# Kernel tuning notes

Measured on AMD Instinct MI355X. Metric: run time of the kernel, lower is better.

The kernel has to match this reference:

```python
import jax, jax.numpy as jnp
import numpy as np

VOCAB = 32000
EMB = 512
HID = 512
MAX_LEN = 32
SOS = 1
PAD = 0


def setup_inputs() -> dict:
    key = jax.random.key(0)
    ks = jax.random.split(key, 9)
    s = 1.0 / np.sqrt(HID)
    emb = jax.random.normal(ks[0], (VOCAB, EMB), jnp.float32)
    emb = emb.at[PAD].set(0.0)  # padding_idx row is zeros
    return {
        "encoder_hidden": jax.random.normal(ks[1], (1, 64, HID), jnp.float32),
        "encoder_c": jax.random.normal(ks[2], (1, 64, HID), jnp.float32),
        "emb": emb,
        "W_ih": jax.random.uniform(ks[3], (4 * HID, EMB), jnp.float32, -s, s),
        "W_hh": jax.random.uniform(ks[4], (4 * HID, HID), jnp.float32, -s, s),
        "b_ih": jax.random.uniform(ks[5], (4 * HID,), jnp.float32, -s, s),
        "b_hh": jax.random.uniform(ks[6], (4 * HID,), jnp.float32, -s, s),
        "fc_w": jax.random.uniform(ks[7], (VOCAB, HID), jnp.float32, -s, s),
        "fc_b": jax.random.uniform(ks[8], (VOCAB,), jnp.float32, -s, s),
    }


def reference(encoder_hidden, encoder_c, emb, W_ih, W_hh, b_ih, b_hh, fc_w, fc_b):
    B = encoder_hidden.shape[1]
    h0 = encoder_hidden[0]  # [B,H] (num_layers == 1)
    c0 = encoder_c[0]
    tok0 = jnp.full((B,), SOS, jnp.int32)
    bias = b_ih + b_hh  # [4H]

    def step(carry, _):
        tok, h, c = carry
        x = emb[tok]  # [B,E] embedding gather
        gates = x @ W_ih.T + h @ W_hh.T + bias  # [B,4H]
        i, f, g, o = jnp.split(gates, 4, axis=-1)  # torch gate order i,f,g,o
        c = jax.nn.sigmoid(f) * c + jax.nn.sigmoid(i) * jnp.tanh(g)
        h = jax.nn.sigmoid(o) * jnp.tanh(c)
        logp = jax.nn.log_softmax(h @ fc_w.T + fc_b, axis=-1)  # [B,V]
        tok_next = jnp.argmax(logp, axis=-1).astype(jnp.int32)  # greedy topk(k=1)
        return (tok_next, h, c), logp

    (_, hT, _), logps = jax.lax.scan(step, (tok0, h0, c0), None, length=MAX_LEN + 1)
    decoder_outputs = jnp.transpose(logps, (1, 0, 2))  # [B, T, V]
    decoder_hidden = hT[None]  # [1, B, H]
    return decoder_outputs, decoder_hidden
```

## Files before the change

kernel.cpp:

```cpp
#include <hip/hip_runtime.h>
#include <math.h>

#define VOCABN 32000
#define HIDN 512
#define BN 64
#define TSTEPS 33
#define OUTROWS (TSTEPS * VOCABN)
#define NVBLK 1000
#define NVT 2000
#define GSLICE 8

typedef float f4 __attribute__((ext_vector_type(4)));
typedef __bf16 bf16x8 __attribute__((ext_vector_type(8)));
typedef unsigned short u16x8 __attribute__((ext_vector_type(8)));

__device__ __forceinline__ unsigned short f2bf_rn(float f) {
    unsigned int u = __builtin_bit_cast(unsigned int, f);
    u += 0x7FFFu + ((u >> 16) & 1u);
    return (unsigned short)(u >> 16);
}
__device__ __forceinline__ float bfbits2f(unsigned short s) {
    unsigned int u = ((unsigned int)s) << 16;
    return __builtin_bit_cast(float, u);
}
__device__ __forceinline__ float sigf(float x) { return 1.f / (1.f + expf(-x)); }
__device__ __forceinline__ void olmerge(float& m, float& s, int& idx,
                                        float mo, float so, int io) {
    float M = fmaxf(m, mo);
    s = s * __expf(m - M) + so * __expf(mo - M);
    idx = (mo > m) ? io : ((mo == m) ? (io < idx ? io : idx) : idx);
    m = M;
}

__global__ __launch_bounds__(256) void k_init(const float* __restrict__ eh,
                                              const float* __restrict__ ec,
                                              float* __restrict__ h,
                                              float* __restrict__ c,
                                              int* __restrict__ tok) {
    int i = blockIdx.x * 256 + threadIdx.x;
    if (i < BN * HIDN) { h[i] = eh[i]; c[i] = ec[i]; }
    if (i < BN) tok[i] = 1;
}

__global__ __launch_bounds__(256) void k_conv(const float* __restrict__ fc_w,
                                              unsigned short* __restrict__ whiP,
                                              unsigned short* __restrict__ wloP) {
    const int vt = blockIdx.x;
    const int tid = threadIdx.x;
    #pragma unroll
    for (int i = 0; i < 4; ++i) {
        const int s = tid + 256 * i;
        const int kc = s >> 6, lane = s & 63;
        const int v = vt * 16 + (lane & 15);
        const int k = kc * 32 + (lane >> 4) * 8;
        const float* src = fc_w + (size_t)v * 512 + k;
        f4 a = *(const f4*)src;
        f4 b = *(const f4*)(src + 4);
        u16x8 hi, lo;
        #pragma unroll
        for (int e = 0; e < 4; ++e) {
            unsigned short ha = f2bf_rn(a[e]);
            hi[e] = ha; lo[e] = f2bf_rn(a[e] - bfbits2f(ha));
            unsigned short hb = f2bf_rn(b[e]);
            hi[4 + e] = hb; lo[4 + e] = f2bf_rn(b[e] - bfbits2f(hb));
        }
        const size_t o = ((size_t)(vt * 16 + kc) * 64 + lane) * 8;
        *(u16x8*)&whiP[o] = hi;
        *(u16x8*)&wloP[o] = lo;
    }
}

__global__ __launch_bounds__(256) void k_gates(const float* __restrict__ W_ih,
                                               const float* __restrict__ W_hh,
                                               const float* __restrict__ emb,
                                               const float* __restrict__ h,
                                               const int* __restrict__ tok,
                                               float* __restrict__ part) {
    __shared__ float w_s[64][68];
    __shared__ float x_s[64][68];
    const int tid = threadIdx.x;
    const int j0 = (blockIdx.x & 31) * 64;
    const int ks = blockIdx.x >> 5;
    const int k0 = ks * 128;
    const int tx = tid & 15;
    const int ty = tid >> 4;
    const int r  = tid >> 2;
    const int cq = (tid & 3) * 16;

    float acc[4][4];
    #pragma unroll
    for (int i = 0; i < 4; ++i)
        #pragma unroll
        for (int j = 0; j < 4; ++j) acc[i][j] = 0.f;

    for (int kk = 0; kk < 128; kk += 64) {
        const int k = k0 + kk;
        __syncthreads();
        {
            const float* src = (k < 512) ? (W_ih + (size_t)(j0 + r) * 512 + k + cq)
                                         : (W_hh + (size_t)(j0 + r) * 512 + (k - 512) + cq);
            const f4* s4 = (const f4*)src;
            f4* d4 = (f4*)&w_s[r][cq];
            d4[0] = s4[0]; d4[1] = s4[1]; d4[2] = s4[2]; d4[3] = s4[3];
        }
        {
            const float* src = (k < 512) ? (emb + (size_t)tok[r] * 512 + k + cq)
                                         : (h + (size_t)r * 512 + (k - 512) + cq);
            const f4* s4 = (const f4*)src;
            f4* d4 = (f4*)&x_s[r][cq];
            d4[0] = s4[0]; d4[1] = s4[1]; d4[2] = s4[2]; d4[3] = s4[3];
        }
        __syncthreads();
        #pragma unroll 4
        for (int c4 = 0; c4 < 64; c4 += 4) {
            f4 wv[4], xv[4];
            #pragma unroll
            for (int jj = 0; jj < 4; ++jj) wv[jj] = *(const f4*)&w_s[16 * jj + tx][c4];
            #pragma unroll
            for (int bb = 0; bb < 4; ++bb) xv[bb] = *(const f4*)&x_s[16 * bb + ty][c4];
            #pragma unroll
            for (int e = 0; e < 4; ++e)
                #pragma unroll
                for (int bb = 0; bb < 4; ++bb)
                    #pragma unroll
                    for (int jj = 0; jj < 4; ++jj)
                        acc[bb][jj] += xv[bb][e] * wv[jj][e];
        }
    }
    #pragma unroll
    for (int bb = 0; bb < 4; ++bb) {
        const int b = 16 * bb + ty;
        #pragma unroll
        for (int jj = 0; jj < 4; ++jj)
            part[((size_t)(ks * 64 + b)) * 2048 + j0 + 16 * jj + tx] = acc[bb][jj];
    }
}

__global__ __launch_bounds__(256) void k_cell(const float* __restrict__ part,
                                              const float* __restrict__ b_ih,
                                              const float* __restrict__ b_hh,
                                              float* __restrict__ h,
                                              float* __restrict__ c,
                                              unsigned short* __restrict__ hhi,
                                              unsigned short* __restrict__ hlo) {
    const int e = blockIdx.x * 256 + threadIdx.x;
    const int b = e >> 9, u = e & 511;
    float g[4];
    #pragma unroll
    for (int gi = 0; gi < 4; ++gi) {
        const int j = gi * 512 + u;
        float s = b_ih[j] + b_hh[j];
        #pragma unroll
        for (int ks = 0; ks < GSLICE; ++ks) s += part[((size_t)(ks * 64 + b)) * 2048 + j];
        g[gi] = s;
    }
    const float ig = sigf(g[0]);
    const float fg = sigf(g[1]);
    const float gg = tanhf(g[2]);
    const float og = sigf(g[3]);
    const float cn = fg * c[e] + ig * gg;
    const float hn = og * tanhf(cn);
    c[e] = cn;
    h[e] = hn;
    const unsigned short hi = f2bf_rn(hn);
    hhi[e] = hi;
    hlo[e] = f2bf_rn(hn - bfbits2f(hi));
}

__global__ __launch_bounds__(256, 4) void k_logits(const unsigned short* __restrict__ whiP,
                                                   const unsigned short* __restrict__ wloP,
                                                   const float* __restrict__ fc_b,
                                                   const unsigned short* __restrict__ hhi,
                                                   const unsigned short* __restrict__ hlo,
                                                   float* __restrict__ outrow,
                                                   float* __restrict__ pm,
                                                   float* __restrict__ ps,
                                                   int* __restrict__ pi) {
    __shared__ float sacc[2][16][64];
    __shared__ float red_m[128];
    __shared__ float red_s[128];
    __shared__ int   red_i[128];

    const int tid  = threadIdx.x;
    const int w    = tid >> 6;
    const int lane = tid & 63;
    const int li   = lane & 15;
    const int lg   = lane >> 4;
    const int vtl  = w >> 1;
    const int kh   = w & 1;
    const int vt   = blockIdx.x * 2 + vtl;

    f4 acc[4];
    #pragma unroll
    for (int bf = 0; bf < 4; ++bf) acc[bf] = (f4){0.f, 0.f, 0.f, 0.f};

    const unsigned short* Ah = whiP + (size_t)vt * 8192 + kh * 4096 + lane * 8;
    const unsigned short* Al = wloP + (size_t)vt * 8192 + kh * 4096 + lane * 8;
    int boff[4];
    #pragma unroll
    for (int bf = 0; bf < 4; ++bf) boff[bf] = (li + 16 * bf) * 512 + kh * 256 + lg * 8;

    #pragma unroll 4
    for (int kc = 0; kc < 8; ++kc) {
        bf16x8 Avh = *(const bf16x8*)(Ah + kc * 512);
        bf16x8 Avl = *(const bf16x8*)(Al + kc * 512);
        #pragma unroll
        for (int bf = 0; bf < 4; ++bf) {
            bf16x8 Bh = *(const bf16x8*)&hhi[boff[bf] + kc * 32];
            bf16x8 Bl = *(const bf16x8*)&hlo[boff[bf] + kc * 32];
            acc[bf] = __builtin_amdgcn_mfma_f32_16x16x32_bf16(Avh, Bh, acc[bf], 0, 0, 0);
            acc[bf] = __builtin_amdgcn_mfma_f32_16x16x32_bf16(Avl, Bh, acc[bf], 0, 0, 0);
            acc[bf] = __builtin_amdgcn_mfma_f32_16x16x32_bf16(Avh, Bl, acc[bf], 0, 0, 0);
        }
    }

    if (kh == 1) {
        #pragma unroll
        for (int bf = 0; bf < 4; ++bf)
            #pragma unroll
            for (int rg = 0; rg < 4; ++rg)
                sacc[vtl][bf * 4 + rg][lane] = acc[bf][rg];
    }
    __syncthreads();

    if (kh == 0) {
        #pragma unroll
        for (int bf = 0; bf < 4; ++bf)
            #pragma unroll
            for (int rg = 0; rg < 4; ++rg)
                acc[bf][rg] += sacc[vtl][bf * 4 + rg][lane];

        const int vbase = vt * 16;
        const f4 bias = *(const f4*)&fc_b[vbase + lg * 4];

        #pragma unroll
        for (int bf = 0; bf < 4; ++bf) {
            f4 x = acc[bf] + bias;
            acc[bf] = x;
            const int b = li + 16 * bf;
            *(f4*)&outrow[(size_t)b * OUTROWS + vbase + lg * 4] = x;
        }

        #pragma unroll
        for (int bf = 0; bf < 4; ++bf) {
            float m = -1e30f; int idx = 0;
            #pragma unroll
            for (int rg = 0; rg < 4; ++rg) {
                float x = acc[bf][rg];
                if (x > m) { m = x; idx = vbase + lg * 4 + rg; }
            }
            float s = 0.f;
            #pragma unroll
            for (int rg = 0; rg < 4; ++rg) s += __expf(acc[bf][rg] - m);
            #pragma unroll
            for (int off = 16; off <= 32; off <<= 1) {
                float mo = __shfl_xor(m, off);
                float so = __shfl_xor(s, off);
                int   io = __shfl_xor(idx, off);
                olmerge(m, s, idx, mo, so, io);
            }
            if (lg == 0) {
                red_m[vtl * 64 + li + 16 * bf] = m;
                red_s[vtl * 64 + li + 16 * bf] = s;
                red_i[vtl * 64 + li + 16 * bf] = idx;
            }
        }
    }
    __syncthreads();
    if (tid < 64) {
        float m = red_m[tid]; float s = red_s[tid]; int idx = red_i[tid];
        olmerge(m, s, idx, red_m[64 + tid], red_s[64 + tid], red_i[64 + tid]);
        pm[blockIdx.x * 64 + tid] = m;
        ps[blockIdx.x * 64 + tid] = s;
        pi[blockIdx.x * 64 + tid] = idx;
    }
}

__global__ __launch_bounds__(256) void k_combine(const float* __restrict__ pm,
                                                 const float* __restrict__ ps,
                                                 const int* __restrict__ pi,
                                                 int* __restrict__ tok,
                                                 float* __restrict__ Lb, int t) {
    __shared__ float sm[256], ss[256];
    __shared__ int si[256];
    const int b = blockIdx.x;
    const int tid = threadIdx.x;
    float m = -1e30f, s = 0.f; int idx = 0;
    for (int blk = tid; blk < NVBLK; blk += 256)
        olmerge(m, s, idx, pm[blk * 64 + b], ps[blk * 64 + b], pi[blk * 64 + b]);
    sm[tid] = m; ss[tid] = s; si[tid] = idx;
    __syncthreads();
    for (int st = 128; st; st >>= 1) {
        if (tid < st) {
            float m0 = sm[tid], s0 = ss[tid]; int i0 = si[tid];
            olmerge(m0, s0, i0, sm[tid + st], ss[tid + st], si[tid + st]);
            sm[tid] = m0; ss[tid] = s0; si[tid] = i0;
        }
        __syncthreads();
    }
    if (tid == 0) { tok[b] = si[0]; Lb[t * 64 + b] = sm[0] + logf(ss[0]); }
}

__global__ __launch_bounds__(256) void k_sub(float* __restrict__ out,
                                             const float* __restrict__ Lb) {
    const int N4 = BN * OUTROWS / 4;
    for (int i4 = blockIdx.x * 256 + threadIdx.x; i4 < N4; i4 += gridDim.x * 256) {
        const int i = i4 * 4;
        const int b = i / OUTROWS;
        const int rem = i - b * OUTROWS;
        const int t = rem / VOCABN;
        f4 x = *(const f4*)&out[i];
        const float L = Lb[t * 64 + b];
        x[0] -= L; x[1] -= L; x[2] -= L; x[3] -= L;
        *(f4*)&out[i] = x;
    }
}

__global__ __launch_bounds__(256) void k_copyh(const float* __restrict__ h,
                                               float* __restrict__ dst) {
    int i = blockIdx.x * 256 + threadIdx.x;
    if (i < BN * HIDN) dst[i] = h[i];
}

__global__ __launch_bounds__(256) void k_logits_f32(const float* __restrict__ fc_w,
                                                    const float* __restrict__ fc_b,
                                                    const float* __restrict__ h,
                                                    float* __restrict__ outrow) {
    __shared__ float w_s[64][68];
    __shared__ float h_s[64][68];
    const int tid = threadIdx.x;
    const int v0 = blockIdx.x * 64;
    const int tx = tid & 15;
    const int ty = tid >> 4;
    const int r  = tid >> 2;
    const int cq = (tid & 3) * 16;

    float acc[4][4];
    #pragma unroll
    for (int i = 0; i < 4; ++i)
        #pragma unroll
        for (int j = 0; j < 4; ++j) acc[i][j] = 0.f;

    for (int k = 0; k < 512; k += 64) {
        __syncthreads();
        {
            const f4* s4 = (const f4*)(fc_w + (size_t)(v0 + r) * 512 + k + cq);
            f4* d4 = (f4*)&w_s[r][cq];
            d4[0] = s4[0]; d4[1] = s4[1]; d4[2] = s4[2]; d4[3] = s4[3];
        }
        {
            const f4* s4 = (const f4*)(h + (size_t)r * 512 + k + cq);
            f4* d4 = (f4*)&h_s[r][cq];
            d4[0] = s4[0]; d4[1] = s4[1]; d4[2] = s4[2]; d4[3] = s4[3];
        }
        __syncthreads();
        #pragma unroll 4
        for (int c4 = 0; c4 < 64; c4 += 4) {
            f4 wv[4], hv[4];
            #pragma unroll
            for (int vv = 0; vv < 4; ++vv) wv[vv] = *(const f4*)&w_s[16 * vv + tx][c4];
            #pragma unroll
            for (int bb = 0; bb < 4; ++bb) hv[bb] = *(const f4*)&h_s[16 * bb + ty][c4];
            #pragma unroll
            for (int e = 0; e < 4; ++e)
                #pragma unroll
                for (int bb = 0; bb < 4; ++bb)
                    #pragma unroll
                    for (int vv = 0; vv < 4; ++vv)
                        acc[bb][vv] += hv[bb][e] * wv[vv][e];
        }
    }
    float bias[4];
    #pragma unroll
    for (int vv = 0; vv < 4; ++vv) bias[vv] = fc_b[v0 + 16 * vv + tx];
    #pragma unroll
    for (int bb = 0; bb < 4; ++bb) {
        const int b = 16 * bb + ty;
        #pragma unroll
        for (int vv = 0; vv < 4; ++vv)
            outrow[(size_t)b * OUTROWS + v0 + 16 * vv + tx] = acc[bb][vv] + bias[vv];
    }
}

__global__ __launch_bounds__(1024) void k_softmax(float* __restrict__ outrow,
                                                  int* __restrict__ tok) {
    const int b = blockIdx.x, tid = threadIdx.x;
    float* row = outrow + (size_t)b * OUTROWS;
    __shared__ float sm[1024];
    __shared__ int si[1024];

    float m = -1e30f; int mi = 0;
    for (int v = tid; v < VOCABN; v += 1024) {
        float x = row[v];
        if (x > m) { m = x; mi = v; }
    }
    sm[tid] = m; si[tid] = mi;
    __syncthreads();
    for (int s = 512; s; s >>= 1) {
        if (tid < s) {
            float xo = sm[tid + s]; int io = si[tid + s];
            if (xo > sm[tid] || (xo == sm[tid] && io < si[tid])) { sm[tid] = xo; si[tid] = io; }
        }
        __syncthreads();
    }
    const float M = sm[0];
    const int ami = si[0];
    __syncthreads();

    float sum = 0.f;
    for (int v = tid; v < VOCABN; v += 1024) sum += __expf(row[v] - M);
    sm[tid] = sum;
    __syncthreads();
    for (int s = 512; s; s >>= 1) {
        if (tid < s) sm[tid] += sm[tid + s];
        __syncthreads();
    }
    const float L = M + logf(sm[0]);
    if (tid == 0) tok[b] = ami;

    for (int v = tid; v < VOCABN; v += 1024) row[v] = row[v] - L;
}

extern "C" void kernel_launch(void* const* d_in, const int* in_sizes, int n_in,
                              void* d_out, int out_size, void* d_ws, size_t ws_size,
                              hipStream_t stream) {
    const float* enc_h = (const float*)d_in[0];
    const float* enc_c = (const float*)d_in[1];
    const float* emb   = (const float*)d_in[2];
    const float* W_ih  = (const float*)d_in[3];
    const float* W_hh  = (const float*)d_in[4];
    const float* b_ih  = (const float*)d_in[5];
    const float* b_hh  = (const float*)d_in[6];
    const float* fc_w  = (const float*)d_in[7];
    const float* fc_b  = (const float*)d_in[8];
    float* out = (float*)d_out;

    char* cur = (char*)d_ws;
    float* h    = (float*)cur;            cur += 32768 * 4;
    float* c    = (float*)cur;            cur += 32768 * 4;
    float* part = (float*)cur;            cur += (size_t)GSLICE * 64 * 2048 * 4;
    unsigned short* hhi = (unsigned short*)cur; cur += 32768 * 2;
    unsigned short* hlo = (unsigned short*)cur; cur += 32768 * 2;
    float* pm   = (float*)cur;            cur += (size_t)NVBLK * 64 * 4;
    float* ps   = (float*)cur;            cur += (size_t)NVBLK * 64 * 4;
    int*   pi   = (int*)cur;              cur += (size_t)NVBLK * 64 * 4;
    float* Lb   = (float*)cur;            cur += TSTEPS * 64 * 4;
    int*   tok  = (int*)cur;              cur += 64 * 4;
    unsigned short* whiP = (unsigned short*)cur; cur += (size_t)NVT * 8192 * 2;
    unsigned short* wloP = (unsigned short*)cur; cur += (size_t)NVT * 8192 * 2;
    const size_t NEED = (size_t)(cur - (char*)d_ws);

    if (ws_size >= NEED) {
        k_conv<<<NVT, 256, 0, stream>>>(fc_w, whiP, wloP);
        k_init<<<128, 256, 0, stream>>>(enc_h, enc_c, h, c, tok);
        for (int t = 0; t < TSTEPS; ++t) {
            k_gates<<<32 * GSLICE, 256, 0, stream>>>(W_ih, W_hh, emb, h, tok, part);
            k_cell<<<128, 256, 0, stream>>>(part, b_ih, b_hh, h, c, hhi, hlo);
            float* outrow = out + (size_t)t * VOCABN;
            k_logits<<<NVBLK, 256, 0, stream>>>(whiP, wloP, fc_b, hhi, hlo, outrow, pm, ps, pi);
            k_combine<<<64, 256, 0, stream>>>(pm, ps, pi, tok, Lb, t);
        }
        k_sub<<<2048, 256, 0, stream>>>(out, Lb);
        k_copyh<<<128, 256, 0, stream>>>(h, out + (size_t)BN * OUTROWS);
    } else {
        k_init<<<128, 256, 0, stream>>>(enc_h, enc_c, h, c, tok);
        for (int t = 0; t < TSTEPS; ++t) {
            k_gates<<<32 * GSLICE, 256, 0, stream>>>(W_ih, W_hh, emb, h, tok, part);
            k_cell<<<128, 256, 0, stream>>>(part, b_ih, b_hh, h, c, hhi, hlo);
            float* outrow = out + (size_t)t * VOCABN;
            k_logits_f32<<<500, 256, 0, stream>>>(fc_w, fc_b, h, outrow);
            k_softmax<<<64, 1024, 0, stream>>>(outrow, tok);
        }
        k_copyh<<<128, 256, 0, stream>>>(h, out + (size_t)BN * OUTROWS);
    }
}
```

Measured before the change: 1.943 ms.

## Fuse previous-step log-softmax normalization into next logits kernel

The separate full-output pass that subtracts the log-sum-exp from every logit is removed. Instead, each step's logits kernel also normalizes the previous step's row, using the L values the combine kernel already wrote, and a small kernel handles only the last step. The logits stores and the fused read-modify-write use nontemporal hints so the large output does not pollute the cache. This removes one full read and write pass over the roughly 270 MB output, at the cost of extra memory traffic inside each latency-bound logits launch.

```diff
diff --git a/kernel.cpp b/kernel.cpp
--- a/kernel.cpp
+++ b/kernel.cpp
@@ -175,7 +175,9 @@
                                                    float* __restrict__ outrow,
                                                    float* __restrict__ pm,
                                                    float* __restrict__ ps,
-                                                   int* __restrict__ pi) {
+                                                   int* __restrict__ pi,
+                                                   const float* __restrict__ Lprev,
+                                                   float* __restrict__ outprev) {
     __shared__ float sacc[2][16][64];
     __shared__ float red_m[128];
     __shared__ float red_s[128];
@@ -238,7 +240,7 @@
             f4 x = acc[bf] + bias;
             acc[bf] = x;
             const int b = li + 16 * bf;
-            *(f4*)&outrow[(size_t)b * OUTROWS + vbase + lg * 4] = x;
+            __builtin_nontemporal_store(x, (f4*)&outrow[(size_t)b * OUTROWS + vbase + lg * 4]);
         }
 
         #pragma unroll
@@ -273,6 +275,20 @@
         pm[blockIdx.x * 64 + tid] = m;
         ps[blockIdx.x * 64 + tid] = s;
         pi[blockIdx.x * 64 + tid] = idx;
+    }
+
+    if (Lprev) {
+        const int v0 = blockIdx.x * 32;
+        const int b  = tid >> 2;
+        const int q  = tid & 3;
+        const float L = Lprev[b];
+        float* rowp = outprev + (size_t)b * OUTROWS + v0 + q * 4;
+        f4 x0 = __builtin_nontemporal_load((const f4*)rowp);
+        f4 x1 = __builtin_nontemporal_load((const f4*)(rowp + 16));
+        x0[0] -= L; x0[1] -= L; x0[2] -= L; x0[3] -= L;
+        x1[0] -= L; x1[1] -= L; x1[2] -= L; x1[3] -= L;
+        __builtin_nontemporal_store(x0, (f4*)rowp);
+        __builtin_nontemporal_store(x1, (f4*)(rowp + 16));
     }
 }
 
@@ -301,18 +317,19 @@
     if (tid == 0) { tok[b] = si[0]; Lb[t * 64 + b] = sm[0] + logf(ss[0]); }
 }
 
-__global__ __launch_bounds__(256) void k_sub(float* __restrict__ out,
-                                             const float* __restrict__ Lb) {
-    const int N4 = BN * OUTROWS / 4;
-    for (int i4 = blockIdx.x * 256 + threadIdx.x; i4 < N4; i4 += gridDim.x * 256) {
+__global__ __launch_bounds__(256) void k_sub_last(float* __restrict__ out,
+                                                  const float* __restrict__ Lb) {
+    const int N4 = BN * VOCABN / 4;
+    int i4 = blockIdx.x * 256 + threadIdx.x;
+    if (i4 < N4) {
         const int i = i4 * 4;
-        const int b = i / OUTROWS;
-        const int rem = i - b * OUTROWS;
-        const int t = rem / VOCABN;
-        f4 x = *(const f4*)&out[i];
-        const float L = Lb[t * 64 + b];
+        const int b = i / VOCABN;
+        const int v = i - b * VOCABN;
+        float* p = out + (size_t)b * OUTROWS + (size_t)(TSTEPS - 1) * VOCABN + v;
+        const float L = Lb[(TSTEPS - 1) * 64 + b];
+        f4 x = *(const f4*)p;
         x[0] -= L; x[1] -= L; x[2] -= L; x[3] -= L;
-        *(f4*)&out[i] = x;
+        *(f4*)p = x;
     }
 }
 
@@ -457,10 +474,12 @@
             k_gates<<<32 * GSLICE, 256, 0, stream>>>(W_ih, W_hh, emb, h, tok, part);
             k_cell<<<128, 256, 0, stream>>>(part, b_ih, b_hh, h, c, hhi, hlo);
             float* outrow = out + (size_t)t * VOCABN;
-            k_logits<<<NVBLK, 256, 0, stream>>>(whiP, wloP, fc_b, hhi, hlo, outrow, pm, ps, pi);
+            const float* Lprev = (t > 0) ? (Lb + (size_t)(t - 1) * 64) : nullptr;
+            k_logits<<<NVBLK, 256, 0, stream>>>(whiP, wloP, fc_b, hhi, hlo, outrow,
+                                                pm, ps, pi, Lprev, outrow - VOCABN);
             k_combine<<<64, 256, 0, stream>>>(pm, ps, pi, tok, Lb, t);
         }
-        k_sub<<<2048, 256, 0, stream>>>(out, Lb);
+        k_sub_last<<<(BN * VOCABN / 4 + 255) / 256, 256, 0, stream>>>(out, Lb);
         k_copyh<<<128, 256, 0, stream>>>(h, out + (size_t)BN * OUTROWS);
     } else {
         k_init<<<128, 256, 0, stream>>>(enc_h, enc_c, h, c, tok);
```

Result: no change. 1.976 ms (+1.7%).
